# Kernel tuning notes

Measured on AMD Instinct MI355X. Metric: run time of the kernel, lower is better.

## Reference

```python
import jax, jax.numpy as jnp
import numpy as np

B, N, D = 64, 256, 768
ITER_STEPS = 1


def _linear_w(key, out_d, in_d):
    s = 1.0 / np.sqrt(in_d)
    return jax.random.uniform(key, (out_d, in_d), jnp.float32, -s, s)


def setup_inputs() -> dict:
    key = jax.random.key(0)
    ks = jax.random.split(key, 16)
    node = jax.random.normal(ks[0], (B, N, D), jnp.float32)
    node_mask = jnp.ones((B, N), jnp.int32)
    argument_graph = jax.random.randint(ks[1], (B, N, N), 0, 2, jnp.int32)
    punctuation_graph = jax.random.randint(ks[2], (B, N, N), 0, 2, jnp.int32)
    inp = {
        "node": node,
        "node_mask": node_mask,
        "argument_graph": argument_graph,
        "punctuation_graph": punctuation_graph,
        # node-relatedness scorer: Linear(D, 1, bias=True)
        "Wq": _linear_w(ks[3], 1, D),
        "bq": jnp.zeros((1,), jnp.float32),
        # self node fc: Linear(D, D, bias=True)
        "Ws": _linear_w(ks[4], D, D),
        "bs": jnp.zeros((D,), jnp.float32),
        # 8 relation projections, Linear(D, D, bias=False)
        "Wa": _linear_w(ks[5], D, D),
        "Wp": _linear_w(ks[6], D, D),
        "Wap": _linear_w(ks[7], D, D),
        "Wpp": _linear_w(ks[8], D, D),
        "Wa2": _linear_w(ks[9], D, D),
        "Wp2": _linear_w(ks[10], D, D),
        "Wap2": _linear_w(ks[11], D, D),
        "Wpp2": _linear_w(ks[12], D, D),
    }
    return inp


def reference(node, node_mask, argument_graph, punctuation_graph,
              Wq, bq, Ws, bs, Wa, Wp, Wap, Wpp, Wa2, Wp2, Wap2, Wpp2):
    f32 = jnp.float32
    mask = node_mask.astype(f32)                      # [B, N]
    n = node.shape[1]
    eye = jnp.eye(n, dtype=f32)
    # dd_graph: node_mask outer product with zeroed diagonal
    dd = mask[:, None, :] * mask[:, :, None] * (1.0 - eye)   # [B, N, N]
    g_a = dd * argument_graph.astype(f32)
    g_p = dd * punctuation_graph.astype(f32)
    # reverse directed edges
    g_ar = dd * jnp.swapaxes(g_a, 1, 2)
    g_pr = dd * jnp.swapaxes(g_p, 1, 2)
    neigh = g_a.sum(-1) + g_p.sum(-1) + g_ar.sum(-1) + g_pr.sum(-1)  # [B, N]
    denom = jnp.where(neigh >= 1.0, neigh, 1.0)

    all_weight = []
    for _ in range(ITER_STEPS):
        # (1) node relatedness
        dw = jax.nn.sigmoid(jnp.einsum('bnd,od->bno', node, Wq) + bq)[..., 0]  # [B, N]
        all_weight.append(dw)
        self_info = jnp.einsum('bnd,ed->bne', node, Ws) + bs

        def msg(g, W):
            # node_weight: broadcast dw over rows, zero where no edge
            nw = dw[:, None, :] * g                    # [B, N, N]
            proj = jnp.einsum('bnd,ed->bne', node, W)  # [B, N, D]
            return jnp.matmul(nw, proj)                # [B, N, D]

        agg = (msg(g_a, Wa) + msg(g_p, Wp) + msg(g_ar, Wap) + msg(g_pr, Wpp)
               + msg(g_a, Wa2) + msg(g_p, Wp2) + msg(g_ar, Wap2) + msg(g_pr, Wpp2))
        agg = agg / denom[..., None]
        # (3) node update
        node = jax.nn.relu(self_info + agg)

    all_weight = jnp.stack(all_weight, axis=1)  # [B, steps, N]
    return node, all_weight
```

## Files before the change

kernel.cpp:

```cpp
#include <hip/hip_runtime.h>
#include <hip/hip_bf16.h>
#include <math.h>

typedef __bf16 bf16;
typedef unsigned char u8;
typedef unsigned long long ull;
typedef __bf16 bf16x8 __attribute__((ext_vector_type(8)));
typedef float f32x4 __attribute__((ext_vector_type(4)));

#define BB 64
#define NN 256
#define DD 768
#define MM (BB*NN)
#define KP 1024
#define WSZ (DD*DD)
#define TL 144


__device__ __forceinline__ void async16(const void* g, void* l) {
  __builtin_amdgcn_global_load_lds((__attribute__((address_space(1))) void*)g,
                                   (__attribute__((address_space(3))) void*)l,
                                   16, 0, 0);
}

__device__ __forceinline__ void stage_tile(const bf16* gsrc, int ld, char* ldst,
                                           int wv, int lane) {
#pragma unroll
  for (int cc = 0; cc < 2; ++cc) {
    int c = wv * 2 + cc;
    int row = c * 16 + (lane >> 2);
    int col = (lane & 3) * 8;
    async16(gsrc + (size_t)row * ld + col, ldst + c * 1024);
  }
}

__device__ __forceinline__ void mma_step(const char* lA, const char* lB,
                                         f32x4 acc[4][4], int lane, int wr, int wc) {
  bf16x8 af[4], bfr[4];
  int rbase = wr * 64 + (lane & 15);
  int cbase = wc * 64 + (lane & 15);
  int ko = (lane >> 4) * 8;
#pragma unroll
  for (int r = 0; r < 4; ++r)
    af[r] = *(const bf16x8*)(lA + (((rbase + r * 16) * 32) + ko) * 2);
#pragma unroll
  for (int c = 0; c < 4; ++c)
    bfr[c] = *(const bf16x8*)(lB + (((cbase + c * 16) * 32) + ko) * 2);
#pragma unroll
  for (int r = 0; r < 4; ++r)
#pragma unroll
    for (int c = 0; c < 4; ++c)
      acc[r][c] = __builtin_amdgcn_mfma_f32_16x16x32_bf16(af[r], bfr[c], acc[r][c], 0, 0, 0);
}

__device__ __forceinline__ void mma_step_fp8t(const char* lA, const char* lB,
                                              f32x4 acc[4][4], int lane, int wr, int wc) {
  long af[4], bfr[4];
  int koq = (lane >> 4) * 1024;
  int mA = (wr * 64 + (lane & 15)) * 8;
  int mB = (wc * 64 + (lane & 15)) * 8;
#pragma unroll
  for (int r = 0; r < 4; ++r)
    af[r] = *(const long*)(lA + koq + mA + r * 128);
#pragma unroll
  for (int c = 0; c < 4; ++c)
    bfr[c] = *(const long*)(lB + koq + mB + c * 128);
#pragma unroll
  for (int r = 0; r < 4; ++r)
#pragma unroll
    for (int c = 0; c < 4; ++c)
      acc[r][c] = __builtin_amdgcn_mfma_f32_16x16x32_fp8_fp8(af[r], bfr[c], acc[r][c], 0, 0, 0);
}

__device__ __forceinline__ void k_step64(const bf16* Ab, int lda, const bf16* Bb, int ldb,
                                         char* smem, f32x4 acc[4][4],
                                         int wv, int lane, int wr, int wc) {
  char* lA0 = smem;
  char* lA1 = smem + 8192;
  char* lB0 = smem + 16384;
  char* lB1 = smem + 24576;
  __syncthreads();
  stage_tile(Ab, lda, lA0, wv, lane);
  stage_tile(Ab + 32, lda, lA1, wv, lane);
  stage_tile(Bb, ldb, lB0, wv, lane);
  stage_tile(Bb + 32, ldb, lB1, wv, lane);
  __builtin_amdgcn_s_waitcnt(0);
  __syncthreads();
  mma_step(lA0, lB0, acc, lane, wr, wc);
  mma_step(lA1, lB1, acc, lane, wr, wc);
}

__device__ __forceinline__ unsigned pack4(float a, float b, float c, float d) {
  int w = 0;
  w = __builtin_amdgcn_cvt_pk_fp8_f32(a, b, w, false);
  w = __builtin_amdgcn_cvt_pk_fp8_f32(c, d, w, true);
  return (unsigned)w;
}

__global__ void k_pre(const float* __restrict__ node, const float* __restrict__ Wq,
                      const float* __restrict__ bq, bf16* __restrict__ node_bf,
                      float* __restrict__ dw, float* __restrict__ allw,
                      float* __restrict__ neigh,
                      const float* __restrict__ Ws,
                      const float* __restrict__ Wa, const float* __restrict__ Wp,
                      const float* __restrict__ Wap, const float* __restrict__ Wpp,
                      const float* __restrict__ Wa2, const float* __restrict__ Wp2,
                      const float* __restrict__ Wap2, const float* __restrict__ Wpp2,
                      bf16* __restrict__ Wcat4, bf16* __restrict__ Ws_bf) {
  if (blockIdx.x < MM / 4) {
    int lane = threadIdx.x & 63, wv = threadIdx.x >> 6;
    int row = blockIdx.x * 4 + wv;
    const float* nr = node + (size_t)row * DD;
    bf16* nb = node_bf + (size_t)row * DD;
    float s = 0.f;
#pragma unroll
    for (int k = 0; k < DD / 64; ++k) {
      int idx = lane + k * 64;
      float v = nr[idx];
      nb[idx] = (bf16)v;
      s += v * Wq[idx];
    }
#pragma unroll
    for (int off = 32; off; off >>= 1) s += __shfl_down(s, off);
    if (lane == 0) {
      float z = s + bq[0];
      float d = 1.f / (1.f + expf(-z));
      dw[row] = d;
      allw[row] = d;
      neigh[row] = 0.f;
    }
  } else {
    int i = (blockIdx.x - MM / 4) * 256 + threadIdx.x;
    Ws_bf[i] = (bf16)Ws[i];
    Wcat4[i]           = (bf16)(Wa[i] + Wa2[i]);
    Wcat4[i + WSZ]     = (bf16)(Wp[i] + Wp2[i]);
    Wcat4[i + 2 * WSZ] = (bf16)(Wap[i] + Wap2[i]);
    Wcat4[i + 3 * WSZ] = (bf16)(Wpp[i] + Wpp2[i]);
  }
}

__device__ __forceinline__ void store_tiled(u8* base, int tile, int kin, int m, uint4 v) {
  size_t o = (size_t)tile * 4096 + (size_t)((kin >> 3) * 1024 + m * 8);
  *(ull*)(base + o)        = ((ull)v.y << 32) | v.x;
  *(ull*)(base + o + 1024) = ((ull)v.w << 32) | v.z;
}

__global__ void k_graph(const int* __restrict__ mask, const int* __restrict__ arg,
                        const int* __restrict__ pun, const float* __restrict__ dw,
                        u8* __restrict__ g8, float* __restrict__ neigh) {
  __shared__ float la[64][65];
  __shared__ float lp[64][65];
  __shared__ float msk[256];
  __shared__ float dwv[256];
  int tid = threadIdx.x;
  int bi = blockIdx.x;
  int b = bi >> 4, it = (bi >> 2) & 3, jt = bi & 3;
  int i0 = it * 64, j0 = jt * 64;
  msk[tid] = (float)mask[b * NN + tid];
  dwv[tid] = dw[b * NN + tid];
  __syncthreads();
  int ir = tid >> 2, c4 = (tid & 3) * 16;
  int i = i0 + ir;
  float mi = msk[i];
  size_t gb = (size_t)b * NN * NN;
  const int* ap = arg + gb + (size_t)i * NN + j0 + c4;
  const int* pp = pun + gb + (size_t)i * NN + j0 + c4;
  float va[16], vp[16];
  float racc = 0.f;
#pragma unroll
  for (int k = 0; k < 16; ++k) {
    int j = j0 + c4 + k;
    float dd = (i == j) ? 0.f : mi * msk[j];
    float ga = dd * (float)ap[k];
    float gp = dd * (float)pp[k];
    la[ir][c4 + k] = ga;
    lp[ir][c4 + k] = gp;
    float w = dwv[j];
    va[k] = w * ga;
    vp[k] = w * gp;
    racc += ga + gp;
  }
  uint4 oa, op;
#pragma unroll
  for (int g = 0; g < 4; ++g) {
    (&oa.x)[g] = pack4(va[g*4], va[g*4+1], va[g*4+2], va[g*4+3]);
    (&op.x)[g] = pack4(vp[g*4], vp[g*4+1], vp[g*4+2], vp[g*4+3]);
  }
  {
    int tR = (b * 2 + (i >> 7)) * 32;
    int K0 = j0 + c4;
    store_tiled(g8, tR + (K0 >> 5),       K0 & 31, i & 127, oa);
    store_tiled(g8, tR + 8 + (K0 >> 5),   K0 & 31, i & 127, op);
  }
  racc += __shfl_xor(racc, 1);
  racc += __shfl_xor(racc, 2);
  if ((tid & 3) == 0) atomicAdd(&neigh[b * NN + i], racc);
  __syncthreads();
  int jr = ir, ic4 = c4;
  float cacc = 0.f;
#pragma unroll
  for (int k = 0; k < 16; ++k) {
    float ga = la[ic4 + k][jr];
    float gp = lp[ic4 + k][jr];
    float w = dwv[i0 + ic4 + k];
    va[k] = w * ga;
    vp[k] = w * gp;
    cacc += ga + gp;
  }
#pragma unroll
  for (int g = 0; g < 4; ++g) {
    (&oa.x)[g] = pack4(va[g*4], va[g*4+1], va[g*4+2], va[g*4+3]);
    (&op.x)[g] = pack4(vp[g*4], vp[g*4+1], vp[g*4+2], vp[g*4+3]);
  }
  {
    int row = j0 + jr;
    int tR = (b * 2 + (row >> 7)) * 32;
    int K2 = i0 + ic4;
    store_tiled(g8, tR + 16 + (K2 >> 5),  K2 & 31, row & 127, oa);
    store_tiled(g8, tR + 24 + (K2 >> 5),  K2 & 31, row & 127, op);
  }
  cacc += __shfl_xor(cacc, 1);
  cacc += __shfl_xor(cacc, 2);
  if ((tid & 3) == 0) atomicAdd(&neigh[b * NN + j0 + jr], cacc);
}

__global__ __launch_bounds__(256) void k_proj(const bf16* __restrict__ node_bf,
                                              const bf16* __restrict__ Wcat4,
                                              u8* __restrict__ p8) {
  __shared__ __align__(16) char smem[32768];
  int tid = threadIdx.x, lane = tid & 63, wv = tid >> 6, wr = wv >> 1, wc = wv & 1;
  int m0 = blockIdx.x * 128;
  int n0 = blockIdx.y * 128;
  const bf16* Ab = node_bf + (size_t)m0 * DD;
  const bf16* Bb = Wcat4 + (size_t)n0 * DD;
  f32x4 z = {0.f, 0.f, 0.f, 0.f};
  f32x4 acc[4][4];
#pragma unroll
  for (int r = 0; r < 4; ++r)
#pragma unroll
    for (int c = 0; c < 4; ++c) acc[r][c] = z;
  for (int k0 = 0; k0 < DD; k0 += 64)
    k_step64(Ab + k0, DD, Bb + k0, DD, smem, acc, wv, lane, wr, wc);
  __syncthreads();
  int b = m0 >> 8, j0 = m0 & 255;
  int X = n0 / DD, e0 = n0 - X * DD;
  u8* tb = (u8*)smem;
#pragma unroll
  for (int r = 0; r < 4; ++r)
#pragma unroll
    for (int c = 0; c < 4; ++c) {
      int n = wc * 64 + c * 16 + (lane & 15);
      int m = wr * 64 + r * 16 + ((lane >> 4) << 2);
      *(unsigned*)(tb + n * TL + m) =
          pack4(acc[r][c][0], acc[r][c][1], acc[r][c][2], acc[r][c][3]);
    }
  __syncthreads();
  int tR = (b * 6 + (e0 >> 7)) * 32 + X * 8;
#pragma unroll
  for (int t = 0; t < 4; ++t) {
    int row = t * 32 + (tid >> 3);
    int col = (tid & 7) * 16;
    uint4 v = *(const uint4*)(tb + row * TL + col);
    int K = j0 + col;
    store_tiled(p8, tR + (K >> 5), K & 31, row, v);
  }
}

__global__ __launch_bounds__(256) void k_agg(const u8* __restrict__ g8,
                                             const u8* __restrict__ p8,
                                             const bf16* __restrict__ node_bf,
                                             const bf16* __restrict__ Ws_bf,
                                             const float* __restrict__ neigh,
                                             const float* __restrict__ bs,
                                             float* __restrict__ out) {
  __shared__ __align__(16) char smem[32768];
  int tid = threadIdx.x, lane = tid & 63, wv = tid >> 6, wr = wv >> 1, wc = wv & 1;
  int l = blockIdx.x;
  int xcd = l & 7, idx = l >> 3;
  int b = (idx / 12) * 8 + xcd;
  int t = idx % 12;
  int i0 = (t / 6) * 128, e0 = (t % 6) * 128;
  f32x4 z = {0.f, 0.f, 0.f, 0.f};
  f32x4 acc[4][4];
#pragma unroll
  for (int r = 0; r < 4; ++r)
#pragma unroll
    for (int c = 0; c < 4; ++c) acc[r][c] = z;
  const u8* At = g8 + (size_t)((b * 2 + (i0 >> 7)) * 32) * 4096;
  const u8* Bt = p8 + (size_t)((b * 6 + (e0 >> 7)) * 32) * 4096;
  int lsoff = wv * 1024;
  int goff = lsoff + lane * 16;
  for (int k0 = 0; k0 < KP; k0 += 128) {
    __syncthreads();
#pragma unroll
    for (int s = 0; s < 4; ++s) {
      size_t toff = (size_t)((k0 >> 5) + s) * 4096 + goff;
      async16(At + toff, smem + s * 4096 + lsoff);
      async16(Bt + toff, smem + 16384 + s * 4096 + lsoff);
    }
    __builtin_amdgcn_s_waitcnt(0);
    __syncthreads();
#pragma unroll
    for (int s = 0; s < 4; ++s)
      mma_step_fp8t(smem + s * 4096, smem + 16384 + s * 4096, acc, lane, wr, wc);
  }
  int rowb = i0 + wr * 64 + (lane >> 4) * 4;
#pragma unroll
  for (int r = 0; r < 4; ++r)
#pragma unroll
    for (int q = 0; q < 4; ++q) {
      float rd = 1.f / fmaxf(neigh[b * NN + rowb + r * 16 + q], 1.f);
#pragma unroll
      for (int c = 0; c < 4; ++c) acc[r][c][q] *= rd;
    }
  const bf16* Ab2 = node_bf + (size_t)(b * NN + i0) * DD;
  const bf16* Bb2 = Ws_bf + (size_t)e0 * DD;
  for (int k0 = 0; k0 < DD; k0 += 64)
    k_step64(Ab2 + k0, DD, Bb2 + k0, DD, smem, acc, wv, lane, wr, wc);
  int colb = e0 + wc * 64 + (lane & 15);
#pragma unroll
  for (int c = 0; c < 4; ++c) {
    int col = colb + c * 16;
    float bv = bs[col];
#pragma unroll
    for (int r = 0; r < 4; ++r)
#pragma unroll
      for (int q = 0; q < 4; ++q) {
        int m = b * NN + rowb + r * 16 + q;
        out[(size_t)m * DD + col] = fmaxf(acc[r][c][q] + bv, 0.f);
      }
  }
}

extern "C" void kernel_launch(void* const* d_in, const int* in_sizes, int n_in,
                              void* d_out, int out_size, void* d_ws, size_t ws_size,
                              hipStream_t stream) {
  const float* node = (const float*)d_in[0];
  const int* mask   = (const int*)d_in[1];
  const int* arg    = (const int*)d_in[2];
  const int* pun    = (const int*)d_in[3];
  const float* Wq   = (const float*)d_in[4];
  const float* bq   = (const float*)d_in[5];
  const float* Ws   = (const float*)d_in[6];
  const float* bs   = (const float*)d_in[7];
  const float* Wa   = (const float*)d_in[8];
  const float* Wp   = (const float*)d_in[9];
  const float* Wap  = (const float*)d_in[10];
  const float* Wpp  = (const float*)d_in[11];
  const float* Wa2  = (const float*)d_in[12];
  const float* Wp2  = (const float*)d_in[13];
  const float* Wap2 = (const float*)d_in[14];
  const float* Wpp2 = (const float*)d_in[15];

  float* out  = (float*)d_out;
  float* allw = out + (size_t)MM * DD;

  char* ws = (char*)d_ws;
  bf16* node_bf = (bf16*)ws;
  float* dw     = (float*)(ws + 25165824);
  float* neigh  = (float*)(ws + 25231360);
  bf16* Wcat4   = (bf16*)(ws + 25296896);
  bf16* Ws_bf   = (bf16*)(ws + 30015488);
  u8*   g8      = (u8*)(ws + 31195136);
  u8*   p8      = (u8*)(ws + 47972352);
  (void)ws_size; (void)in_sizes; (void)n_in; (void)out_size;

  k_pre<<<MM / 4 + WSZ / 256, 256, 0, stream>>>(node, Wq, bq, node_bf, dw, allw,
                                                neigh, Ws, Wa, Wp, Wap, Wpp,
                                                Wa2, Wp2, Wap2, Wpp2, Wcat4, Ws_bf);
  k_graph<<<BB * 16, 256, 0, stream>>>(mask, arg, pun, dw, g8, neigh);
  k_proj<<<dim3(128, 24), 256, 0, stream>>>(node_bf, Wcat4, p8);
  k_agg<<<12 * BB, 256, 0, stream>>>(g8, p8, node_bf, Ws_bf, neigh, bs, out);
}
```

Baseline: 325.3 us.

## Rewrite projection GEMM as 256x256-tile, 4-stage async LDS pipeline

Replaces the 128x128 projection GEMM with 512-thread blocks computing 256x256 tiles. Operands are staged by a four-deep ring of async global-to-LDS loads, with vmcnt-based waits, swizzled LDS addressing and raised wave priority around the MFMA burst. Blocks are remapped so a batch stays on one XCD. The aim is more operand reuse and less exposed load latency. In exchange it needs 128KB of LDS per block and more accumulator registers, which limits occupancy.

```diff
diff --git a/kernel.cpp b/kernel.cpp
--- a/kernel.cpp
+++ b/kernel.cpp
@@ -14,7 +14,8 @@
 #define MM (BB*NN)
 #define KP 1024
 #define WSZ (DD*DD)
-#define TL 144
+#define TL2 272
+#define AROW2 196608
 
 
 __device__ __forceinline__ void async16(const void* g, void* l) {
@@ -224,45 +225,113 @@
   if ((tid & 3) == 0) atomicAdd(&neigh[b * NN + j0 + jr], cacc);
 }
 
-__global__ __launch_bounds__(256) void k_proj(const bf16* __restrict__ node_bf,
-                                              const bf16* __restrict__ Wcat4,
-                                              u8* __restrict__ p8) {
-  __shared__ __align__(16) char smem[32768];
-  int tid = threadIdx.x, lane = tid & 63, wv = tid >> 6, wr = wv >> 1, wc = wv & 1;
-  int m0 = blockIdx.x * 128;
-  int n0 = blockIdx.y * 128;
-  const bf16* Ab = node_bf + (size_t)m0 * DD;
-  const bf16* Bb = Wcat4 + (size_t)n0 * DD;
+template<int VM>
+__device__ __forceinline__ void wait_vm() {
+  if constexpr (VM == 12)     asm volatile("s_waitcnt vmcnt(12)" ::: "memory");
+  else if constexpr (VM == 8) asm volatile("s_waitcnt vmcnt(8)"  ::: "memory");
+  else if constexpr (VM == 4) asm volatile("s_waitcnt vmcnt(4)"  ::: "memory");
+  else                        asm volatile("s_waitcnt vmcnt(0)"  ::: "memory");
+}
+
+template<int P, int VM, bool STAGE>
+__device__ __forceinline__ void proj_phase(int t, char* smem, int wvoff,
+                                           const char* gA, const char* gB,
+                                           int aoff, int boff, f32x4 (&acc)[8][4]) {
+  if constexpr (STAGE) {
+    int u = t + 3;
+    char* D = smem + ((P + 3) & 3) * 32768 + wvoff;
+    const char* sA = gA + u * 64;
+    const char* sB = gB + u * 64;
+    async16(sA,         D);
+    async16(sA + AROW2, D + 8192);
+    async16(sB,         D + 16384);
+    async16(sB + AROW2, D + 24576);
+  }
+  wait_vm<VM>();
+  __builtin_amdgcn_s_barrier();
+  __builtin_amdgcn_sched_barrier(0);
+  const char* L = smem + P * 32768;
+  bf16x8 af[8], bfr[4];
+#pragma unroll
+  for (int r = 0; r < 8; ++r) af[r] = *(const bf16x8*)(L + aoff + r * 1024);
+#pragma unroll
+  for (int c = 0; c < 4; ++c) bfr[c] = *(const bf16x8*)(L + boff + c * 1024);
+  __builtin_amdgcn_s_setprio(1);
+#pragma unroll
+  for (int r = 0; r < 8; ++r)
+#pragma unroll
+    for (int c = 0; c < 4; ++c)
+      acc[r][c] = __builtin_amdgcn_mfma_f32_16x16x32_bf16(af[r], bfr[c], acc[r][c], 0, 0, 0);
+  __builtin_amdgcn_s_setprio(0);
+  __builtin_amdgcn_sched_barrier(0);
+  __builtin_amdgcn_s_barrier();
+}
+
+__global__ __launch_bounds__(512, 2) void k_proj(const bf16* __restrict__ node_bf,
+                                                 const bf16* __restrict__ Wcat4,
+                                                 u8* __restrict__ p8) {
+  __shared__ __align__(16) char smem[131072];
+  int tid = threadIdx.x, lane = tid & 63, wv = tid >> 6;
+  int wr = wv >> 2, wc = wv & 3;
+  int l = blockIdx.x, xcd = l & 7, idx = l >> 3;
+  int b = (idx / 12) * 8 + xcd;
+  int nt = idx % 12;
+  int n0 = nt * 256;
+  int m0 = b * 256;
+  int srcS = (tid & 3) ^ ((tid >> 3) & 3);
+  const char* gA = (const char*)node_bf + (size_t)m0 * 1536 + (tid >> 2) * 1536 + srcS * 16;
+  const char* gB = (const char*)Wcat4  + (size_t)n0 * 1536 + (tid >> 2) * 1536 + srcS * 16;
+  int wvoff = wv * 1024;
+  int sSwR = ((lane >> 4) ^ (((lane & 15) >> 1) & 3)) << 4;
+  int aoff = (wr * 128 + (lane & 15)) * 64 + sSwR;
+  int boff = 16384 + (wc * 64 + (lane & 15)) * 64 + sSwR;
   f32x4 z = {0.f, 0.f, 0.f, 0.f};
-  f32x4 acc[4][4];
-#pragma unroll
-  for (int r = 0; r < 4; ++r)
+  f32x4 acc[8][4];
+#pragma unroll
+  for (int r = 0; r < 8; ++r)
 #pragma unroll
     for (int c = 0; c < 4; ++c) acc[r][c] = z;
-  for (int k0 = 0; k0 < DD; k0 += 64)
-    k_step64(Ab + k0, DD, Bb + k0, DD, smem, acc, wv, lane, wr, wc);
-  __syncthreads();
-  int b = m0 >> 8, j0 = m0 & 255;
-  int X = n0 / DD, e0 = n0 - X * DD;
+#pragma unroll
+  for (int u = 0; u < 3; ++u) {
+    char* D = smem + u * 32768 + wvoff;
+    const char* sA = gA + u * 64;
+    const char* sB = gB + u * 64;
+    async16(sA,         D);
+    async16(sA + AROW2, D + 8192);
+    async16(sB,         D + 16384);
+    async16(sB + AROW2, D + 24576);
+  }
+  for (int tt = 0; tt < 20; tt += 4) {
+    proj_phase<0, 12, true>(tt + 0, smem, wvoff, gA, gB, aoff, boff, acc);
+    proj_phase<1, 12, true>(tt + 1, smem, wvoff, gA, gB, aoff, boff, acc);
+    proj_phase<2, 12, true>(tt + 2, smem, wvoff, gA, gB, aoff, boff, acc);
+    proj_phase<3, 12, true>(tt + 3, smem, wvoff, gA, gB, aoff, boff, acc);
+  }
+  proj_phase<0, 12, true >(20, smem, wvoff, gA, gB, aoff, boff, acc);
+  proj_phase<1,  8, false>(21, smem, wvoff, gA, gB, aoff, boff, acc);
+  proj_phase<2,  4, false>(22, smem, wvoff, gA, gB, aoff, boff, acc);
+  proj_phase<3,  0, false>(23, smem, wvoff, gA, gB, aoff, boff, acc);
+  __syncthreads();
   u8* tb = (u8*)smem;
-#pragma unroll
-  for (int r = 0; r < 4; ++r)
+  int X = n0 / DD, e0 = n0 % DD;
+#pragma unroll
+  for (int r = 0; r < 8; ++r)
 #pragma unroll
     for (int c = 0; c < 4; ++c) {
       int n = wc * 64 + c * 16 + (lane & 15);
-      int m = wr * 64 + r * 16 + ((lane >> 4) << 2);
-      *(unsigned*)(tb + n * TL + m) =
+      int m = wr * 128 + r * 16 + ((lane >> 4) << 2);
+      *(unsigned*)(tb + n * TL2 + m) =
           pack4(acc[r][c][0], acc[r][c][1], acc[r][c][2], acc[r][c][3]);
     }
   __syncthreads();
-  int tR = (b * 6 + (e0 >> 7)) * 32 + X * 8;
-#pragma unroll
-  for (int t = 0; t < 4; ++t) {
-    int row = t * 32 + (tid >> 3);
-    int col = (tid & 7) * 16;
-    uint4 v = *(const uint4*)(tb + row * TL + col);
-    int K = j0 + col;
-    store_tiled(p8, tR + (K >> 5), K & 31, row, v);
+#pragma unroll
+  for (int t2 = 0; t2 < 8; ++t2) {
+    int erow = t2 * 32 + (tid & 31);
+    int col = (tid >> 5) * 16;
+    uint4 v = *(const uint4*)(tb + erow * TL2 + col);
+    int e = e0 + erow;
+    int tR = (b * 6 + (e >> 7)) * 32 + X * 8;
+    store_tiled(p8, tR + (col >> 5), col & 31, e & 127, v);
   }
 }
 
@@ -369,6 +438,6 @@
                                                 neigh, Ws, Wa, Wp, Wap, Wpp,
                                                 Wa2, Wp2, Wap2, Wpp2, Wcat4, Ws_bf);
   k_graph<<<BB * 16, 256, 0, stream>>>(mask, arg, pun, dw, g8, neigh);
-  k_proj<<<dim3(128, 24), 256, 0, stream>>>(node_bf, Wcat4, p8);
+  k_proj<<<768, 512, 0, stream>>>(node_bf, Wcat4, p8);
   k_agg<<<12 * BB, 256, 0, stream>>>(g8, p8, node_bf, Ws_bf, neigh, bs, out);
 }
```

Measured after the change: 319.6 us. About the same (-1.7%).

## Pipeline k_proj GEMM with triple-buffered async LDS loads and XCD-aware tiling

Applied to the files above, without the earlier changes.

Rewrites the projection GEMM main loop as a fully unrolled 24-phase pipeline. Each phase issues async global-to-LDS loads three stages ahead into a triple-buffered 48KB shared region, double-buffers register fragments, and runs the MFMAs under raised wave priority. LDS reads use a swizzled layout, and the grid is flattened to 1D with a remap so M tiles spread across XCDs and share the weight tiles in L2. The larger LDS footprint and launch bound of 3 blocks per CU may limit occupancy, and the hand-written waitcnt counts have to match the load ordering exactly.

```diff
diff --git a/kernel.cpp b/kernel.cpp
--- a/kernel.cpp
+++ b/kernel.cpp
@@ -224,27 +224,117 @@
   if ((tid & 3) == 0) atomicAdd(&neigh[b * NN + j0 + jr], cacc);
 }
 
-__global__ __launch_bounds__(256) void k_proj(const bf16* __restrict__ node_bf,
-                                              const bf16* __restrict__ Wcat4,
-                                              u8* __restrict__ p8) {
-  __shared__ __align__(16) char smem[32768];
-  int tid = threadIdx.x, lane = tid & 63, wv = tid >> 6, wr = wv >> 1, wc = wv & 1;
-  int m0 = blockIdx.x * 128;
-  int n0 = blockIdx.y * 128;
-  const bf16* Ab = node_bf + (size_t)m0 * DD;
-  const bf16* Bb = Wcat4 + (size_t)n0 * DD;
+template<int T>
+__device__ __forceinline__ void proj_ph(char* smem, int stoff,
+                                        const char* gA, const char* gB,
+                                        int aoff, int boff,
+                                        bf16x8 (&ca)[4], bf16x8 (&cb)[4],
+                                        bf16x8 (&na)[4], bf16x8 (&nb)[4],
+                                        f32x4 (&acc)[4][4]) {
+  if constexpr (T <= 21)      asm volatile("s_waitcnt vmcnt(4)" ::: "memory");
+  else if constexpr (T == 22) asm volatile("s_waitcnt vmcnt(0)" ::: "memory");
+  __builtin_amdgcn_s_barrier();
+  __builtin_amdgcn_sched_barrier(0);
+  if constexpr (T + 3 < 24) {
+    constexpr int B = (T % 3) * 16384;
+    const char* sA = gA + (T + 3) * 64;
+    const char* sB = gB + (T + 3) * 64;
+    char* D = smem + B + stoff;
+    async16(sA,         D);
+    async16(sA + 98304, D + 4096);
+    async16(sB,         D + 8192);
+    async16(sB + 98304, D + 12288);
+  }
+  if constexpr (T + 1 < 24) {
+    const char* L = smem + ((T + 1) % 3) * 16384;
+#pragma unroll
+    for (int r = 0; r < 4; ++r) na[r] = *(const bf16x8*)(L + aoff + r * 1024);
+#pragma unroll
+    for (int c = 0; c < 4; ++c) nb[c] = *(const bf16x8*)(L + boff + c * 1024);
+  }
+  __builtin_amdgcn_s_setprio(1);
+#pragma unroll
+  for (int r = 0; r < 4; ++r)
+#pragma unroll
+    for (int c = 0; c < 4; ++c)
+      acc[r][c] = __builtin_amdgcn_mfma_f32_16x16x32_bf16(ca[r], cb[c], acc[r][c], 0, 0, 0);
+  __builtin_amdgcn_s_setprio(0);
+  asm volatile("s_waitcnt lgkmcnt(0)" ::: "memory");
+  __builtin_amdgcn_sched_barrier(0);
+}
+
+__global__ __launch_bounds__(256, 3) void k_proj(const bf16* __restrict__ node_bf,
+                                                 const bf16* __restrict__ Wcat4,
+                                                 u8* __restrict__ p8) {
+  __shared__ __align__(16) char smem[49152];
+  int tid = threadIdx.x, lane = tid & 63, wv = tid >> 6;
+  int wr = wv >> 1, wc = wv & 1;
+  int l = blockIdx.x, xcd = l & 7, idx = l >> 3;
+  int mt = (idx / 24) * 8 + xcd;
+  int nt = idx % 24;
+  int m0 = mt * 128;
+  int n0 = nt * 128;
+  int srcS = (tid & 3) ^ ((tid >> 3) & 3);
+  const char* gA = (const char*)node_bf + (size_t)m0 * 1536 + (tid >> 2) * 1536 + srcS * 16;
+  const char* gB = (const char*)Wcat4  + (size_t)n0 * 1536 + (tid >> 2) * 1536 + srcS * 16;
+  int stoff = wv * 1024;
+  int sSwR = ((lane >> 4) ^ (((lane & 15) >> 1) & 3)) << 4;
+  int aoff = (wr * 64 + (lane & 15)) * 64 + sSwR;
+  int boff = 8192 + (wc * 64 + (lane & 15)) * 64 + sSwR;
   f32x4 z = {0.f, 0.f, 0.f, 0.f};
   f32x4 acc[4][4];
 #pragma unroll
   for (int r = 0; r < 4; ++r)
 #pragma unroll
     for (int c = 0; c < 4; ++c) acc[r][c] = z;
-  for (int k0 = 0; k0 < DD; k0 += 64)
-    k_step64(Ab + k0, DD, Bb + k0, DD, smem, acc, wv, lane, wr, wc);
-  __syncthreads();
+  bf16x8 fa0[4], fb0[4], fa1[4], fb1[4];
+#pragma unroll
+  for (int u = 0; u < 3; ++u) {
+    const char* sA = gA + u * 64;
+    const char* sB = gB + u * 64;
+    char* D = smem + u * 16384 + stoff;
+    async16(sA,         D);
+    async16(sA + 98304, D + 4096);
+    async16(sB,         D + 8192);
+    async16(sB + 98304, D + 12288);
+  }
+  asm volatile("s_waitcnt vmcnt(8)" ::: "memory");
+  __builtin_amdgcn_s_barrier();
+  __builtin_amdgcn_sched_barrier(0);
+#pragma unroll
+  for (int r = 0; r < 4; ++r) fa0[r] = *(const bf16x8*)(smem + aoff + r * 1024);
+#pragma unroll
+  for (int c = 0; c < 4; ++c) fb0[c] = *(const bf16x8*)(smem + boff + c * 1024);
+  asm volatile("s_waitcnt lgkmcnt(0)" ::: "memory");
+  __builtin_amdgcn_sched_barrier(0);
+  proj_ph< 0>(smem, stoff, gA, gB, aoff, boff, fa0, fb0, fa1, fb1, acc);
+  proj_ph< 1>(smem, stoff, gA, gB, aoff, boff, fa1, fb1, fa0, fb0, acc);
+  proj_ph< 2>(smem, stoff, gA, gB, aoff, boff, fa0, fb0, fa1, fb1, acc);
+  proj_ph< 3>(smem, stoff, gA, gB, aoff, boff, fa1, fb1, fa0, fb0, acc);
+  proj_ph< 4>(smem, stoff, gA, gB, aoff, boff, fa0, fb0, fa1, fb1, acc);
+  proj_ph< 5>(smem, stoff, gA, gB, aoff, boff, fa1, fb1, fa0, fb0, acc);
+  proj_ph< 6>(smem, stoff, gA, gB, aoff, boff, fa0, fb0, fa1, fb1, acc);
+  proj_ph< 7>(smem, stoff, gA, gB, aoff, boff, fa1, fb1, fa0, fb0, acc);
+  proj_ph< 8>(smem, stoff, gA, gB, aoff, boff, fa0, fb0, fa1, fb1, acc);
+  proj_ph< 9>(smem, stoff, gA, gB, aoff, boff, fa1, fb1, fa0, fb0, acc);
+  proj_ph<10>(smem, stoff, gA, gB, aoff, boff, fa0, fb0, fa1, fb1, acc);
+  proj_ph<11>(smem, stoff, gA, gB, aoff, boff, fa1, fb1, fa0, fb0, acc);
+  proj_ph<12>(smem, stoff, gA, gB, aoff, boff, fa0, fb0, fa1, fb1, acc);
+  proj_ph<13>(smem, stoff, gA, gB, aoff, boff, fa1, fb1, fa0, fb0, acc);
+  proj_ph<14>(smem, stoff, gA, gB, aoff, boff, fa0, fb0, fa1, fb1, acc);
+  proj_ph<15>(smem, stoff, gA, gB, aoff, boff, fa1, fb1, fa0, fb0, acc);
+  proj_ph<16>(smem, stoff, gA, gB, aoff, boff, fa0, fb0, fa1, fb1, acc);
+  proj_ph<17>(smem, stoff, gA, gB, aoff, boff, fa1, fb1, fa0, fb0, acc);
+  proj_ph<18>(smem, stoff, gA, gB, aoff, boff, fa0, fb0, fa1, fb1, acc);
+  proj_ph<19>(smem, stoff, gA, gB, aoff, boff, fa1, fb1, fa0, fb0, acc);
+  proj_ph<20>(smem, stoff, gA, gB, aoff, boff, fa0, fb0, fa1, fb1, acc);
+  proj_ph<21>(smem, stoff, gA, gB, aoff, boff, fa1, fb1, fa0, fb0, acc);
+  proj_ph<22>(smem, stoff, gA, gB, aoff, boff, fa0, fb0, fa1, fb1, acc);
+  proj_ph<23>(smem, stoff, gA, gB, aoff, boff, fa1, fb1, fa0, fb0, acc);
+  __syncthreads();
+  u8* tb = (u8*)smem;
   int b = m0 >> 8, j0 = m0 & 255;
-  int X = n0 / DD, e0 = n0 - X * DD;
-  u8* tb = (u8*)smem;
+  int X = nt / 6, e0 = (nt % 6) * 128;
 #pragma unroll
   for (int r = 0; r < 4; ++r)
 #pragma unroll
@@ -257,8 +347,8 @@
   __syncthreads();
   int tR = (b * 6 + (e0 >> 7)) * 32 + X * 8;
 #pragma unroll
-  for (int t = 0; t < 4; ++t) {
-    int row = t * 32 + (tid >> 3);
+  for (int t2 = 0; t2 < 4; ++t2) {
+    int row = t2 * 32 + (tid >> 3);
     int col = (tid & 7) * 16;
     uint4 v = *(const uint4*)(tb + row * TL + col);
     int K = j0 + col;
@@ -369,6 +459,6 @@
                                                 neigh, Ws, Wa, Wp, Wap, Wpp,
                                                 Wa2, Wp2, Wap2, Wpp2, Wcat4, Ws_bf);
   k_graph<<<BB * 16, 256, 0, stream>>>(mask, arg, pun, dw, g8, neigh);
-  k_proj<<<dim3(128, 24), 256, 0, stream>>>(node_bf, Wcat4, p8);
+  k_proj<<<3072, 256, 0, stream>>>(node_bf, Wcat4, p8);
   k_agg<<<12 * BB, 256, 0, stream>>>(g8, p8, node_bf, Ws_bf, neigh, bs, out);
 }
```

Result: slower. 335.6 us (+3.1%).
